# Kernel optimization log

Hardware: AMD Instinct MI355X
Metric: run time of the kernel (lower is better)

## Reference

```python
import jax, jax.numpy as jnp
import numpy as np

B, S, D = 2, 2048, 1024
H, DK = 16, 64          # n_heads, d_kv; inner_dim = H*DK = D
NUM_BUCKETS = 32        # T5 relative_attention_num_buckets
MAX_DIST = 128          # T5 relative_attention_max_distance
SM_SCALE = 1.0 / np.sqrt(H)  # module uses 1/sqrt(n_heads), not 1/sqrt(d_kv)


def setup_inputs() -> dict:
    key = jax.random.key(0)
    ks = jax.random.split(key, 6)
    w = 0.02  # typical init scale for projection weights
    return {
        "hidden_states": jax.random.normal(ks[0], (B, S, D), jnp.float32),
        "Wq": jax.random.normal(ks[1], (D, H * DK), jnp.float32) * w,
        "Wk": jax.random.normal(ks[2], (D, H * DK), jnp.float32) * w,
        "Wv": jax.random.normal(ks[3], (D, H * DK), jnp.float32) * w,
        "Wo": jax.random.normal(ks[4], (H * DK, D), jnp.float32) * w,
        "rel_bias": jax.random.normal(ks[5], (NUM_BUCKETS, H), jnp.float32) * w,
    }


def _relative_position_buckets(qlen, klen):
    """T5 bidirectional relative-position bucketing -> [qlen, klen] int32."""
    ctx = jnp.arange(qlen, dtype=jnp.int32)[:, None]
    mem = jnp.arange(klen, dtype=jnp.int32)[None, :]
    rp = mem - ctx  # relative position
    nb = NUM_BUCKETS // 2  # bidirectional split
    ret = (rp > 0).astype(jnp.int32) * nb
    rpa = jnp.abs(rp)
    max_exact = nb // 2
    is_small = rpa < max_exact
    rpf = jnp.maximum(rpa, 1).astype(jnp.float32)
    large = max_exact + (
        jnp.log(rpf / max_exact) / np.log(MAX_DIST / max_exact) * (nb - max_exact)
    ).astype(jnp.int32)
    large = jnp.minimum(large, nb - 1)
    return ret + jnp.where(is_small, rpa, large)


def reference(hidden_states, Wq, Wk, Wv, Wo, rel_bias):
    b, s, d = hidden_states.shape
    q = (hidden_states @ Wq).reshape(b, s, H, DK)
    k = (hidden_states @ Wk).reshape(b, s, H, DK)
    v = (hidden_states @ Wv).reshape(b, s, H, DK)

    buckets = _relative_position_buckets(s, s)        # [S, S]
    bias = rel_bias[buckets]                          # [S, S, H]
    bias = jnp.transpose(bias, (2, 0, 1))[None]       # [1, H, S, S]

    scores = jnp.einsum("bqhd,bkhd->bhqk", q, k) * SM_SCALE + bias
    attn = jax.nn.softmax(scores, axis=-1)
    out = jnp.einsum("bhqk,bkhd->bqhd", attn, v).reshape(b, s, H * DK)
    return out @ Wo
```

## Files before the change

### kernel.cpp

```cpp
#include <hip/hip_runtime.h>
#include <math.h>


typedef _Float16 f16;
typedef _Float16 f16x4 __attribute__((ext_vector_type(4)));
typedef _Float16 f16x8 __attribute__((ext_vector_type(8)));
typedef float f32x4 __attribute__((ext_vector_type(4)));
typedef float f32x16 __attribute__((ext_vector_type(16)));
typedef unsigned int u32;
typedef u32 u32x4 __attribute__((ext_vector_type(4)));

#define MFMA16(a, b, c) __builtin_amdgcn_mfma_f32_16x16x32_f16((a), (b), (c), 0, 0, 0)
#define MFMA32(a, b, c) __builtin_amdgcn_mfma_f32_32x32x16_f16((a), (b), (c), 0, 0, 0)

static __device__ __forceinline__ float EXP2(float x) {
  float r;
  asm("v_exp_f32 %0, %1" : "=v"(r) : "v"(x));
  return r;
}

static __device__ __forceinline__ u32 pk2(float a, float b) {
  return __builtin_bit_cast(u32, __builtin_amdgcn_cvt_pkrtz(a, b));
}
static __device__ __forceinline__ void swap32(u32& a, u32& b) {
  asm volatile("v_permlane32_swap_b32 %0, %1" : "+v"(a), "+v"(b));
}

__device__ __forceinline__ void gload16(const f16* g, f16* l) {
  __builtin_amdgcn_global_load_lds(
      (const __attribute__((address_space(1))) void*)g,
      (__attribute__((address_space(3))) void*)l, 16, 0, 0);
}


__global__ __launch_bounds__(256) void cast_x_kernel(const float4* __restrict__ x,
                                                     f16x4* __restrict__ xh) {
  int i = blockIdx.x * 256 + threadIdx.x;
  float4 v = x[i];
  f16x4 o;
  o[0] = (f16)v.x; o[1] = (f16)v.y; o[2] = (f16)v.z; o[3] = (f16)v.w;
  xh[i] = o;
}

__global__ void transpose_w_kernel(const float* __restrict__ w0, const float* __restrict__ w1,
                                   const float* __restrict__ w2, const float* __restrict__ w3,
                                   f16* __restrict__ wt) {
  int z = blockIdx.z;
  const float* w = (z == 0) ? w0 : (z == 1) ? w1 : (z == 2) ? w2 : w3;
  float sc = (z == 0) ? 0.36067376022224085f : 1.0f;
  __shared__ float tile[32][33];
  int tx = threadIdx.x, ty = threadIdx.y;
  int kt = blockIdx.x * 32, nt = blockIdx.y * 32;
#pragma unroll
  for (int i = 0; i < 4; ++i)
    tile[ty + i * 8][tx] = w[(size_t)(kt + ty + i * 8) * 1024 + nt + tx];
  __syncthreads();
#pragma unroll
  for (int i = 0; i < 4; ++i)
    wt[((size_t)z * 1024 + nt + ty + i * 8) * 1024 + kt + tx] = (f16)(tile[tx][ty + i * 8] * sc);
}

__global__ __launch_bounds__(256) void bias_kernel(const float* __restrict__ rel_bias,
                                                   f16* __restrict__ bias_rel) {
  int idx = blockIdx.x * 256 + threadIdx.x;
  int h = idx >> 12;
  int r = idx & 4095;
  int rp = r - 2048;
  if (rp < -2047) rp = -2047;
  int bucket = (rp > 0) ? 16 : 0;
  int rpa = (rp < 0) ? -rp : rp;
  if (rpa < 8) {
    bucket += rpa;
  } else {
    int large = 8 + (int)(logf((float)rpa / 8.0f) / logf(16.0f) * 8.0f);
    bucket += (large < 15) ? large : 15;
  }
  bias_rel[idx] = (f16)(rel_bias[bucket * 16 + h] * 1.4426950408889634f);
}

__device__ __forceinline__ void gemm128_core(const f16* __restrict__ A, const f16* __restrict__ Bt,
                                             int mrow, int ncol0, f16* sm ,
                                             f32x4 acc[4][4]) {
  const int t = threadIdx.x;
  const int lane = t & 63, w = t >> 6;
  const int cL = lane & 15, g = lane >> 4;
  const int wr = w >> 1, wc = w & 1;

  const int c0 = w * 128 + lane;
  const int c1 = c0 + 64;
  const int rA0 = c0 >> 2, kA0 = ((c0 & 3) ^ (rA0 & 3)) << 3;
  const int rA1 = c1 >> 2, kA1 = ((c1 & 3) ^ (rA1 & 3)) << 3;
  const f16* gA0 = A + (size_t)(mrow + rA0) * 1024 + kA0;
  const f16* gA1 = A + (size_t)(mrow + rA1) * 1024 + kA1;
  const f16* gB0 = Bt + (size_t)(ncol0 + rA0) * 1024 + kA0;
  const f16* gB1 = Bt + (size_t)(ncol0 + rA1) * 1024 + kA1;
  const int lds0 = (w * 2) * 512, lds1 = (w * 2 + 1) * 512;

#define GSTAGE(buf, k0)                            \
  do {                                             \
    f16* s_ = sm + (buf) * 8192;                   \
    gload16(gA0 + (k0), s_ + lds0);                \
    gload16(gA1 + (k0), s_ + lds1);                \
    gload16(gB0 + (k0), s_ + 4096 + lds0);         \
    gload16(gB1 + (k0), s_ + 4096 + lds1);         \
  } while (0)

  GSTAGE(0, 0);
  __syncthreads();
#pragma unroll 2
  for (int ks = 0; ks < 32; ++ks) {
    const int cur = ks & 1;
    if (ks < 31) GSTAGE(cur ^ 1, (ks + 1) * 32);
    const f16* bA = sm + cur * 8192;
    const f16* bB = bA + 4096;
    f16x8 af[4], bf[4];
#pragma unroll
    for (int m = 0; m < 4; ++m) {
      int r = wr * 64 + m * 16 + cL;
      af[m] = *(const f16x8*)&bA[r * 32 + ((g ^ (r & 3)) << 3)];
    }
#pragma unroll
    for (int n = 0; n < 4; ++n) {
      int r = wc * 64 + n * 16 + cL;
      bf[n] = *(const f16x8*)&bB[r * 32 + ((g ^ (r & 3)) << 3)];
    }
#pragma unroll
    for (int m = 0; m < 4; ++m)
#pragma unroll
      for (int n = 0; n < 4; ++n) acc[m][n] = MFMA16(af[m], bf[n], acc[m][n]);
    __syncthreads();
  }
#undef GSTAGE
}

__global__ __launch_bounds__(256) void gemm_qkv_kernel(const f16* __restrict__ Xh,
                                                       const f16* __restrict__ Wt,
                                                       f16* __restrict__ Qh,
                                                       f16* __restrict__ Kh,
                                                       f16* __restrict__ Vt) {
  __shared__ __align__(16) f16 sm[2][8192];
  int mrow = blockIdx.y * 128, ncol0 = blockIdx.x * 128;
  f32x4 acc[4][4] = {};
  gemm128_core(Xh, Wt, mrow, ncol0, &sm[0][0], acc);
  int lane = threadIdx.x & 63, w = threadIdx.x >> 6;
  int cL = lane & 15, g = lane >> 4;
  int wr = w >> 1, wc = w & 1;
  int which = (ncol0 + wc * 64) >> 10;
#pragma unroll
  for (int m = 0; m < 4; ++m) {
#pragma unroll
    for (int n = 0; n < 4; ++n) {
#pragma unroll
      for (int r = 0; r < 4; ++r) {
        int tt = mrow + wr * 64 + m * 16 + g * 4 + r;
        int b = tt >> 11, s = tt & 2047;
        int col = (ncol0 + wc * 64 + n * 16 + cL) & 1023;
        int hh = col >> 6, dk = col & 63;
        f16 val = (f16)acc[m][n][r];
        if (which == 0)
          Qh[(((size_t)b * 16 + hh) * 2048 + s) * 64 + dk] = val;
        else if (which == 1)
          Kh[(((size_t)b * 16 + hh) * 2048 + s) * 64 + dk] = val;
        else
          Vt[(((size_t)b * 16 + hh) * 64 + dk) * 2048 + s] = val;
      }
    }
  }
}

__global__ __launch_bounds__(256) void gemm_out_kernel(const f16* __restrict__ Oh,
                                                       const f16* __restrict__ WoT,
                                                       float* __restrict__ out) {
  __shared__ __align__(16) f16 sm[2][8192];
  int mrow = blockIdx.y * 128, ncol0 = blockIdx.x * 128;
  f32x4 acc[4][4] = {};
  gemm128_core(Oh, WoT, mrow, ncol0, &sm[0][0], acc);
  int lane = threadIdx.x & 63, w = threadIdx.x >> 6;
  int cL = lane & 15, g = lane >> 4;
  int wr = w >> 1, wc = w & 1;
#pragma unroll
  for (int m = 0; m < 4; ++m)
#pragma unroll
    for (int n = 0; n < 4; ++n)
#pragma unroll
      for (int r = 0; r < 4; ++r) {
        int tt = mrow + wr * 64 + m * 16 + g * 4 + r;
        out[(size_t)tt * 1024 + ncol0 + wc * 64 + n * 16 + cL] = acc[m][n][r];
      }
}

__global__ __launch_bounds__(256) void attn_kernel(const f16* __restrict__ Qh,
                                                   const f16* __restrict__ Kh,
                                                   const f16* __restrict__ Vt,
                                                   const f16* __restrict__ bias_rel,
                                                   f16* __restrict__ Oh) {
  __shared__ __align__(16) f16 sKV[2][8192];
  __shared__ __align__(16) f16 sB[2176];
  int bh = blockIdx.y;
  int h = bh & 15, b = bh >> 4;
  int qt = blockIdx.x * 128;
  int t = threadIdx.x;
  int lane = t & 63, wave = t >> 6;
  int lo5 = lane & 31, hi = lane >> 5;
  const size_t bhS = (size_t)bh * 2048;
  const int qrow = qt + wave * 32 + lo5;

  const f16* qp = Qh + (bhS + qrow) * 64 + hi * 8;
  f16x8 qf[4];
#pragma unroll
  for (int m = 0; m < 4; ++m) qf[m] = *(const f16x8*)(qp + 16 * m);

  float cpos = (float)bias_rel[(size_t)h * 4096 + 4095];
  float cneg = (float)bias_rel[(size_t)h * 4096 + 1];

  {
    const float4* gB = (const float4*)(bias_rel + (size_t)h * 4096 + 1920 - qt);
    for (int i = t; i < 272; i += 256) ((float4*)sB)[i] = gB[i];
  }

  const int rK0 = t >> 3, ccK0 = ((t & 7) ^ (rK0 & 7)) << 3;
  const int rK1 = rK0 + 32, ccK1 = ((t & 7) ^ (rK1 & 7)) << 3;
  const f16* gK0 = Kh + (bhS + rK0) * 64 + ccK0;
  const f16* gK1 = Kh + (bhS + rK1) * 64 + ccK1;
  const f16* gV0 = Vt + ((size_t)bh * 64 + rK0) * 2048 + ccK0;
  const f16* gV1 = Vt + ((size_t)bh * 64 + rK1) * 2048 + ccK1;
  const int ldsA = wave * 512, ldsB = wave * 512 + 2048;

#define ASTAGE(buf, key0)                           \
  do {                                              \
    f16* s_ = &sKV[buf][0];                         \
    gload16(gK0 + (size_t)(key0) * 64, s_ + ldsA);  \
    gload16(gK1 + (size_t)(key0) * 64, s_ + ldsB);  \
    gload16(gV0 + (key0), s_ + 4096 + ldsA);        \
    gload16(gV1 + (key0), s_ + 4096 + ldsB);        \
  } while (0)

  f32x16 o0 = {}, o1 = {};
  float m_ = -INFINITY, lsum = 0.f;
  const int sw7 = lo5 & 7;

  ASTAGE(0, 0);
  __syncthreads();
  for (int kt = 0; kt < 32; ++kt) {
    const int cur = kt & 1;
    if (kt < 31) ASTAGE(cur ^ 1, (kt + 1) * 64);
    const int key0 = kt * 64;
    const f16* kb = &sKV[cur][0];
    const f16* vb = kb + 4096;
    const int dkt = key0 - qt;

    f32x16 sa0, sa1;
    if (dkt >= 256 || dkt <= -192) {
      float c = (dkt > 0) ? cpos : cneg;
#pragma unroll
      for (int i = 0; i < 16; ++i) { sa0[i] = c; sa1[i] = c; }
    } else {
      const int bb = key0 + 4 * hi - wave * 32 - lo5 + 128;
#pragma unroll
      for (int i = 0; i < 16; ++i) {
        int pat = (i & 3) + 8 * (i >> 2);
        sa0[i] = (float)sB[bb + pat];
        sa1[i] = (float)sB[bb + 32 + pat];
      }
    }
    const f16* kr0 = kb + lo5 * 64;
    const f16* kr1 = kb + (32 + lo5) * 64;
    __builtin_amdgcn_s_setprio(1);
#pragma unroll
    for (int m = 0; m < 4; ++m) {
      int c = ((2 * m + hi) ^ sw7) << 3;
      sa0 = MFMA32(*(const f16x8*)(kr0 + c), qf[m], sa0);
      sa1 = MFMA32(*(const f16x8*)(kr1 + c), qf[m], sa1);
    }
    __builtin_amdgcn_s_setprio(0);
    float tm[16];
#pragma unroll
    for (int i = 0; i < 16; ++i) tm[i] = fmaxf(sa0[i], sa1[i]);
#pragma unroll
    for (int s2 = 8; s2; s2 >>= 1)
#pragma unroll
      for (int i = 0; i < 8; ++i)
        if (i < s2) tm[i] = fmaxf(tm[i], tm[i + s2]);
    float mx = fmaxf(tm[0], __shfl_xor(tm[0], 32));
    if (__any(mx > m_ + 8.f)) {
      float mn = fmaxf(m_, mx);
      float corr = EXP2(m_ - mn);
      lsum *= corr;
      m_ = mn;
#pragma unroll
      for (int i = 0; i < 16; ++i) { o0[i] *= corr; o1[i] *= corr; }
    }
    float p[16];
    u32 w0, w1, w2, w3, w4, w5, w6, w7;
#pragma unroll
    for (int i = 0; i < 16; ++i) p[i] = EXP2(sa0[i] - m_);
    w0 = pk2(p[0], p[1]);   w1 = pk2(p[2], p[3]);
    w2 = pk2(p[4], p[5]);   w3 = pk2(p[6], p[7]);
    w4 = pk2(p[8], p[9]);   w5 = pk2(p[10], p[11]);
    w6 = pk2(p[12], p[13]); w7 = pk2(p[14], p[15]);
#pragma unroll
    for (int s2 = 8; s2; s2 >>= 1)
#pragma unroll
      for (int i = 0; i < 8; ++i)
        if (i < s2) p[i] += p[i + s2];
    float ls = p[0];
    swap32(w0, w2); swap32(w1, w3); swap32(w4, w6); swap32(w5, w7);
    f16x8 pb0 = __builtin_bit_cast(f16x8, (u32x4){w0, w1, w2, w3});
    f16x8 pb1 = __builtin_bit_cast(f16x8, (u32x4){w4, w5, w6, w7});
#pragma unroll
    for (int i = 0; i < 16; ++i) p[i] = EXP2(sa1[i] - m_);
    w0 = pk2(p[0], p[1]);   w1 = pk2(p[2], p[3]);
    w2 = pk2(p[4], p[5]);   w3 = pk2(p[6], p[7]);
    w4 = pk2(p[8], p[9]);   w5 = pk2(p[10], p[11]);
    w6 = pk2(p[12], p[13]); w7 = pk2(p[14], p[15]);
#pragma unroll
    for (int s2 = 8; s2; s2 >>= 1)
#pragma unroll
      for (int i = 0; i < 8; ++i)
        if (i < s2) p[i] += p[i + s2];
    lsum += ls + p[0];
    swap32(w0, w2); swap32(w1, w3); swap32(w4, w6); swap32(w5, w7);
    f16x8 pb2 = __builtin_bit_cast(f16x8, (u32x4){w0, w1, w2, w3});
    f16x8 pb3 = __builtin_bit_cast(f16x8, (u32x4){w4, w5, w6, w7});
    const f16* vr0 = vb + lo5 * 64;
    const f16* vr1 = vb + (32 + lo5) * 64;
    __builtin_amdgcn_s_setprio(1);
    {
      int c = ((0 + hi) ^ sw7) << 3;
      o0 = MFMA32(*(const f16x8*)(vr0 + c), pb0, o0);
      o1 = MFMA32(*(const f16x8*)(vr1 + c), pb0, o1);
    }
    {
      int c = ((2 + hi) ^ sw7) << 3;
      o0 = MFMA32(*(const f16x8*)(vr0 + c), pb1, o0);
      o1 = MFMA32(*(const f16x8*)(vr1 + c), pb1, o1);
    }
    {
      int c = ((4 + hi) ^ sw7) << 3;
      o0 = MFMA32(*(const f16x8*)(vr0 + c), pb2, o0);
      o1 = MFMA32(*(const f16x8*)(vr1 + c), pb2, o1);
    }
    {
      int c = ((6 + hi) ^ sw7) << 3;
      o0 = MFMA32(*(const f16x8*)(vr0 + c), pb3, o0);
      o1 = MFMA32(*(const f16x8*)(vr1 + c), pb3, o1);
    }
    __builtin_amdgcn_s_setprio(0);
    __syncthreads();
  }
#undef ASTAGE
  lsum += __shfl_xor(lsum, 32);
  float inv = 1.0f / lsum;
  size_t base = ((size_t)b * 2048 + qrow) * 1024 + h * 64 + 4 * hi;
#pragma unroll
  for (int rq = 0; rq < 4; ++rq) {
    f16x4 v0, v1;
#pragma unroll
    for (int j = 0; j < 4; ++j) {
      v0[j] = (f16)(o0[rq * 4 + j] * inv);
      v1[j] = (f16)(o1[rq * 4 + j] * inv);
    }
    *(f16x4*)&Oh[base + 8 * rq] = v0;
    *(f16x4*)&Oh[base + 32 + 8 * rq] = v1;
  }
}


extern "C" void kernel_launch(void* const* d_in, const int* in_sizes, int n_in,
                              void* d_out, int out_size, void* d_ws, size_t ws_size,
                              hipStream_t stream) {
  const float* X = (const float*)d_in[0];
  const float* Wq = (const float*)d_in[1];
  const float* Wk = (const float*)d_in[2];
  const float* Wv = (const float*)d_in[3];
  const float* Wo = (const float*)d_in[4];
  const float* relb = (const float*)d_in[5];

  const size_t MB8 = (size_t)8 << 20;
  if (ws_size < 6 * MB8 + (1 << 19)) return;

  char* ws = (char*)d_ws;
  f16* Xh = (f16*)(ws + 0 * MB8);
  f16* Wt = (f16*)(ws + 1 * MB8);
  f16* Qh = (f16*)(ws + 2 * MB8);
  f16* Kh = (f16*)(ws + 3 * MB8);
  f16* Vt = (f16*)(ws + 4 * MB8);
  f16* Oh = (f16*)(ws + 5 * MB8);
  f16* brel = (f16*)(ws + 6 * MB8);

  cast_x_kernel<<<dim3(4096), dim3(256), 0, stream>>>((const float4*)X, (f16x4*)Xh);
  transpose_w_kernel<<<dim3(32, 32, 4), dim3(32, 8), 0, stream>>>(Wq, Wk, Wv, Wo, Wt);
  bias_kernel<<<dim3(256), dim3(256), 0, stream>>>(relb, brel);
  gemm_qkv_kernel<<<dim3(24, 32), dim3(256), 0, stream>>>(Xh, Wt, Qh, Kh, Vt);
  attn_kernel<<<dim3(16, 32), dim3(256), 0, stream>>>(Qh, Kh, Vt, brel, Oh);
  gemm_out_kernel<<<dim3(8, 32), dim3(256), 0, stream>>>(Oh, Wt + (size_t)3072 * 1024,
                                                         (float*)d_out);
}
```

Measured before the change: 150.1 us.

## Deepen attention K/V pipeline to four LDS buffers with vmcnt waits and remap blocks

```diff
diff --git a/kernel.cpp b/kernel.cpp
--- a/kernel.cpp
+++ b/kernel.cpp
@@ -25,6 +25,12 @@
 static __device__ __forceinline__ void swap32(u32& a, u32& b) {
   asm volatile("v_permlane32_swap_b32 %0, %1" : "+v"(a), "+v"(b));
 }
+
+#define KEEPV8(v8)                                                        \
+  do {                                                                    \
+    u32x4 _t = __builtin_bit_cast(u32x4, (v8));                           \
+    asm volatile("" ::"v"(_t[0]), "v"(_t[1]), "v"(_t[2]), "v"(_t[3]));    \
+  } while (0)
 
 __device__ __forceinline__ void gload16(const f16* g, f16* l) {
   __builtin_amdgcn_global_load_lds(
@@ -194,11 +200,13 @@
                                                    const f16* __restrict__ Vt,
                                                    const f16* __restrict__ bias_rel,
                                                    f16* __restrict__ Oh) {
-  __shared__ __align__(16) f16 sKV[2][8192];
+  __shared__ __align__(16) f16 sKV[4][8192];
   __shared__ __align__(16) f16 sB[2176];
-  int bh = blockIdx.y;
-  int h = bh & 15, b = bh >> 4;
-  int qt = blockIdx.x * 128;
+  const int p = blockIdx.x;
+  const int L = ((p & 7) << 6) + (p >> 3);
+  const int bh = L >> 4;
+  const int qt = (L & 15) << 7;
+  const int h = bh & 15, b = bh >> 4;
   int t = threadIdx.x;
   int lane = t & 63, wave = t >> 6;
   int lo5 = lane & 31, hi = lane >> 5;
@@ -212,6 +220,10 @@
 
   float cpos = (float)bias_rel[(size_t)h * 4096 + 4095];
   float cneg = (float)bias_rel[(size_t)h * 4096 + 1];
+
+#pragma unroll
+  for (int m = 0; m < 4; ++m) KEEPV8(qf[m]);
+  asm volatile("" ::"v"(cpos), "v"(cneg));
 
   {
     const float4* gB = (const float4*)(bias_rel + (size_t)h * 4096 + 1920 - qt);
@@ -240,12 +252,21 @@
   const int sw7 = lo5 & 7;
 
   ASTAGE(0, 0);
-  __syncthreads();
+  ASTAGE(1, 64);
+  asm volatile("s_waitcnt lgkmcnt(0)" ::: "memory");
+
   for (int kt = 0; kt < 32; ++kt) {
-    const int cur = kt & 1;
-    if (kt < 31) ASTAGE(cur ^ 1, (kt + 1) * 64);
+    if (kt < 30) ASTAGE((kt + 2) & 3, (kt + 2) * 64);
+    if (kt < 30)
+      asm volatile("s_waitcnt vmcnt(8)" ::: "memory");
+    else if (kt == 30)
+      asm volatile("s_waitcnt vmcnt(4)" ::: "memory");
+    else
+      asm volatile("s_waitcnt vmcnt(0)" ::: "memory");
+    __builtin_amdgcn_s_barrier();
+
     const int key0 = kt * 64;
-    const f16* kb = &sKV[cur][0];
+    const f16* kb = &sKV[kt & 3][0];
     const f16* vb = kb + 4096;
     const int dkt = key0 - qt;
 
@@ -290,35 +311,35 @@
 #pragma unroll
       for (int i = 0; i < 16; ++i) { o0[i] *= corr; o1[i] *= corr; }
     }
-    float p[16];
+    float pr[16];
     u32 w0, w1, w2, w3, w4, w5, w6, w7;
 #pragma unroll
-    for (int i = 0; i < 16; ++i) p[i] = EXP2(sa0[i] - m_);
-    w0 = pk2(p[0], p[1]);   w1 = pk2(p[2], p[3]);
-    w2 = pk2(p[4], p[5]);   w3 = pk2(p[6], p[7]);
-    w4 = pk2(p[8], p[9]);   w5 = pk2(p[10], p[11]);
-    w6 = pk2(p[12], p[13]); w7 = pk2(p[14], p[15]);
+    for (int i = 0; i < 16; ++i) pr[i] = EXP2(sa0[i] - m_);
+    w0 = pk2(pr[0], pr[1]);   w1 = pk2(pr[2], pr[3]);
+    w2 = pk2(pr[4], pr[5]);   w3 = pk2(pr[6], pr[7]);
+    w4 = pk2(pr[8], pr[9]);   w5 = pk2(pr[10], pr[11]);
+    w6 = pk2(pr[12], pr[13]); w7 = pk2(pr[14], pr[15]);
 #pragma unroll
     for (int s2 = 8; s2; s2 >>= 1)
 #pragma unroll
       for (int i = 0; i < 8; ++i)
-        if (i < s2) p[i] += p[i + s2];
-    float ls = p[0];
+        if (i < s2) pr[i] += pr[i + s2];
+    float ls = pr[0];
     swap32(w0, w2); swap32(w1, w3); swap32(w4, w6); swap32(w5, w7);
     f16x8 pb0 = __builtin_bit_cast(f16x8, (u32x4){w0, w1, w2, w3});
     f16x8 pb1 = __builtin_bit_cast(f16x8, (u32x4){w4, w5, w6, w7});
 #pragma unroll
-    for (int i = 0; i < 16; ++i) p[i] = EXP2(sa1[i] - m_);
-    w0 = pk2(p[0], p[1]);   w1 = pk2(p[2], p[3]);
-    w2 = pk2(p[4], p[5]);   w3 = pk2(p[6], p[7]);
-    w4 = pk2(p[8], p[9]);   w5 = pk2(p[10], p[11]);
-    w6 = pk2(p[12], p[13]); w7 = pk2(p[14], p[15]);
+    for (int i = 0; i < 16; ++i) pr[i] = EXP2(sa1[i] - m_);
+    w0 = pk2(pr[0], pr[1]);   w1 = pk2(pr[2], pr[3]);
+    w2 = pk2(pr[4], pr[5]);   w3 = pk2(pr[6], pr[7]);
+    w4 = pk2(pr[8], pr[9]);   w5 = pk2(pr[10], pr[11]);
+    w6 = pk2(pr[12], pr[13]); w7 = pk2(pr[14], pr[15]);
 #pragma unroll
     for (int s2 = 8; s2; s2 >>= 1)
 #pragma unroll
       for (int i = 0; i < 8; ++i)
-        if (i < s2) p[i] += p[i + s2];
-    lsum += ls + p[0];
+        if (i < s2) pr[i] += pr[i + s2];
+    lsum += ls + pr[0];
     swap32(w0, w2); swap32(w1, w3); swap32(w4, w6); swap32(w5, w7);
     f16x8 pb2 = __builtin_bit_cast(f16x8, (u32x4){w0, w1, w2, w3});
     f16x8 pb3 = __builtin_bit_cast(f16x8, (u32x4){w4, w5, w6, w7});
@@ -346,7 +367,6 @@
       o1 = MFMA32(*(const f16x8*)(vr1 + c), pb3, o1);
     }
     __builtin_amdgcn_s_setprio(0);
-    __syncthreads();
   }
 #undef ASTAGE
   lsum += __shfl_xor(lsum, 32);
@@ -392,7 +412,7 @@
   transpose_w_kernel<<<dim3(32, 32, 4), dim3(32, 8), 0, stream>>>(Wq, Wk, Wv, Wo, Wt);
   bias_kernel<<<dim3(256), dim3(256), 0, stream>>>(relb, brel);
   gemm_qkv_kernel<<<dim3(24, 32), dim3(256), 0, stream>>>(Xh, Wt, Qh, Kh, Vt);
-  attn_kernel<<<dim3(16, 32), dim3(256), 0, stream>>>(Qh, Kh, Vt, brel, Oh);
+  attn_kernel<<<dim3(512), dim3(256), 0, stream>>>(Qh, Kh, Vt, brel, Oh);
   gemm_out_kernel<<<dim3(8, 32), dim3(256), 0, stream>>>(Oh, Wt + (size_t)3072 * 1024,
                                                          (float*)d_out);
 }
```

New measurement: 148.9 us. No clear change (-0.8%).
